# Kernel optimization log

Hardware: AMD Instinct MI355X
Metric: run time of the kernel (lower is better)

The kernel has to match this reference:

```python
import jax, jax.numpy as jnp
import numpy as np

D_MODEL = 1024
NUM_HEADS = 16
D_K = D_MODEL // NUM_HEADS


def setup_inputs() -> dict:
    key = jax.random.key(0)
    ks = jax.random.split(key, 12)
    B, S, D = 2, 2048, D_MODEL
    s = 1.0 / np.sqrt(D)
    inp = {
        "Q": jax.random.normal(ks[0], (B, S, D), jnp.float32),
        "K": jax.random.normal(ks[1], (B, S, D), jnp.float32),
        "V": jax.random.normal(ks[2], (B, S, D), jnp.float32),
        "Wq": jax.random.normal(ks[3], (D, D), jnp.float32) * s,
        "bq": jax.random.normal(ks[4], (D,), jnp.float32) * s,
        "Wk": jax.random.normal(ks[5], (D, D), jnp.float32) * s,
        "bk": jax.random.normal(ks[6], (D,), jnp.float32) * s,
        "Wv": jax.random.normal(ks[7], (D, D), jnp.float32) * s,
        "bv": jax.random.normal(ks[8], (D,), jnp.float32) * s,
        "Wo": jax.random.normal(ks[9], (D, D), jnp.float32) * s,
        "bo": jax.random.normal(ks[10], (D,), jnp.float32) * s,
    }
    return inp


def _split_heads(x, B, S):
    # [B, S, D] -> [B, H, S, d_k]
    return x.reshape(B, S, NUM_HEADS, D_K).transpose(0, 2, 1, 3)


def reference(Q, K, V, Wq, bq, Wk, bk, Wv, bv, Wo, bo):
    B, S, D = Q.shape
    # torch nn.Linear: y = x @ W.T + b
    q = _split_heads(Q @ Wq.T + bq, B, S)
    k = _split_heads(K @ Wk.T + bk, B, S)
    v = _split_heads(V @ Wv.T + bv, B, S)
    scale = 1.0 / np.sqrt(D_K).astype(np.float32)
    # [B, H, S, S] attention scores (materialized, as in the original)
    scores = jnp.einsum('bhqd,bhkd->bhqk', q, k) * scale
    probs = jax.nn.softmax(scores, axis=-1)
    out = jnp.einsum('bhqk,bhkd->bhqd', probs, v)
    out = out.transpose(0, 2, 1, 3).reshape(B, S, D)
    return out @ Wo.T + bo
```

## Files before the change

kernel.cpp:

```cpp
#include <hip/hip_runtime.h>
#include <hip/hip_bf16.h>

#define S_LEN   2048
#define NHEADS  16
#define DKH     64
#define DMODEL  1024
#define NBATCH  2

typedef __bf16 bf16x8 __attribute__((ext_vector_type(8)));
typedef __bf16 bf16x4 __attribute__((ext_vector_type(4)));
typedef float  f32x4  __attribute__((ext_vector_type(4)));

typedef __attribute__((address_space(3))) void       lds_void;
typedef const __attribute__((address_space(1))) void glob_void;

__device__ __forceinline__ void glds16(const void* g, void* l) {
    __builtin_amdgcn_global_load_lds((glob_void*)g, (lds_void*)l, 16, 0, 0);
}

struct CvtArgs {
    const float* src[7];
    __bf16*      dst[7];
    int          n[7];
};

__global__ __launch_bounds__(256)
void cvt_all_k(CvtArgs a)
{
    const int t = blockIdx.y;
    const size_t i = ((size_t)blockIdx.x * 256 + threadIdx.x) * 8;
    if ((int)i >= a.n[t]) return;
    const float* s = a.src[t];
    f32x4 lo = *(const f32x4*)(s + i);
    f32x4 hi = *(const f32x4*)(s + i + 4);
    bf16x8 r;
#pragma unroll
    for (int k = 0; k < 4; ++k) { r[k] = (__bf16)lo[k]; r[4 + k] = (__bf16)hi[k]; }
    *(bf16x8*)(a.dst[t] + i) = r;
}

#define BM 128
#define BN 64
#define BK 32

template<int MODE>
__global__ __launch_bounds__(256)
void gemm_tiled(const __bf16* __restrict__ A, const __bf16* __restrict__ W,
                const float* __restrict__ bias, void* __restrict__ outp,
                int M, int N, int K, float oscale)
{
    __shared__ __align__(16) __bf16 As[BM][BK];
    __shared__ __align__(16) __bf16 Ws[BN][BK];

    const int tid  = threadIdx.x;
    const int lane = tid & 63;
    const int wv   = tid >> 6;
    const int l15  = lane & 15;
    const int quad = lane >> 4;
    const int wm   = wv >> 1;
    const int wn   = wv & 1;

    const int fid = blockIdx.x;
    const int x  = fid & 7;
    const int j  = fid >> 3;
    const int m0 = (x * 4 + (j & 3)) * BM;
    const int n0 = (j >> 2) * BN;

    const int grow = lane >> 2;
    const int gcol = (lane & 3) * 8;
    const __bf16* ag0 = A + (size_t)(m0 + wv * 32 + grow) * K + gcol;
    const __bf16* ag1 = A + (size_t)(m0 + wv * 32 + 16 + grow) * K + gcol;
    const __bf16* wg  = W + (size_t)(n0 + wv * 16 + grow) * K + gcol;
    void* al0 = &As[wv * 32][0];
    void* al1 = &As[wv * 32 + 16][0];
    void* wl  = &Ws[wv * 16][0];

    f32x4 acc[4][2];
#pragma unroll
    for (int i = 0; i < 4; ++i)
#pragma unroll
        for (int jj = 0; jj < 2; ++jj) acc[i][jj] = (f32x4){0.f, 0.f, 0.f, 0.f};

    for (int k0 = 0;;) {
        __syncthreads();
        glds16(ag0 + k0, al0);
        glds16(ag1 + k0, al1);
        glds16(wg + k0, wl);
        __syncthreads();

        bf16x8 af[4], wf[2];
#pragma unroll
        for (int i = 0; i < 4; ++i)
            af[i] = *(const bf16x8*)&As[wm * 64 + i * 16 + l15][quad * 8];
#pragma unroll
        for (int jj = 0; jj < 2; ++jj)
            wf[jj] = *(const bf16x8*)&Ws[wn * 32 + jj * 16 + l15][quad * 8];
#pragma unroll
        for (int i = 0; i < 4; ++i)
#pragma unroll
            for (int jj = 0; jj < 2; ++jj)
                acc[i][jj] = __builtin_amdgcn_mfma_f32_16x16x32_bf16(af[i], wf[jj], acc[i][jj], 0, 0, 0);

        k0 += BK;
        if (k0 >= K) break;
    }

#pragma unroll
    for (int jj = 0; jj < 2; ++jj) {
        const int col = n0 + wn * 32 + jj * 16 + l15;
        const float bv = bias[col];
#pragma unroll
        for (int i = 0; i < 4; ++i) {
#pragma unroll
            for (int r = 0; r < 4; ++r) {
                const int row = m0 + wm * 64 + i * 16 + quad * 4 + r;
                const float v = (acc[i][jj][r] + bv) * oscale;
                if (MODE == 2) {
                    ((float*)outp)[(size_t)row * N + col] = v;
                } else {
                    const int b = row >> 11;
                    const int s = row & (S_LEN - 1);
                    const int h = col >> 6;
                    const int d = col & (DKH - 1);
                    const size_t idx = (MODE == 0)
                        ? ((size_t)(b * NHEADS + h) * S_LEN + s) * DKH + d
                        : ((size_t)(b * NHEADS + h) * DKH + d) * S_LEN + s;
                    ((__bf16*)outp)[idx] = (__bf16)v;
                }
            }
        }
    }
}

__global__ __launch_bounds__(512)
void attn_k(const __bf16* __restrict__ Qh, const __bf16* __restrict__ Kh,
            const __bf16* __restrict__ VhT, __bf16* __restrict__ out)
{
    __shared__ __align__(16) __bf16 Ks[64][72];
    __shared__ __align__(16) __bf16 Vs[64][72];

    const int tid  = threadIdx.x;
    const int lane = tid & 63;
    const int wv   = tid >> 6;
    const int l15  = lane & 15;
    const int quad = lane >> 4;

    const int fid = blockIdx.x;
    const int x  = fid & 7;
    const int j  = fid >> 3;
    const int bh = x * 4 + (j & 3);
    const int q0 = (j >> 2) * 128;
    const int b  = bh >> 4;
    const int h  = bh & (NHEADS - 1);

    const __bf16* Q  = Qh  + (size_t)bh * S_LEN * DKH;
    const __bf16* Kp = Kh  + (size_t)bh * S_LEN * DKH;
    const __bf16* Vt = VhT + (size_t)bh * DKH * S_LEN;

    const int qrow = q0 + wv * 16 + l15;
    const bf16x8 qa0 = *(const bf16x8*)(Q + (size_t)qrow * DKH + quad * 8);
    const bf16x8 qa1 = *(const bf16x8*)(Q + (size_t)qrow * DKH + quad * 8 + 32);

    const int srow = tid >> 3;
    const int scol = (tid & 7) * 8;
    const __bf16* kst = Kp + (size_t)srow * DKH   + scol;
    const __bf16* vst = Vt + (size_t)srow * S_LEN + scol;

    f32x4 oT[4];
#pragma unroll
    for (int jj = 0; jj < 4; ++jj) oT[jj] = (f32x4){0.f, 0.f, 0.f, 0.f};
    float lacc = 0.f;

    bf16x8 kr = *(const bf16x8*)(kst);
    bf16x8 vr = *(const bf16x8*)(vst);

    for (int kt = 0; kt < S_LEN; kt += 64) {
        __syncthreads();
        *(bf16x8*)&Ks[srow][scol] = kr;
        *(bf16x8*)&Vs[srow][scol] = vr;
        __syncthreads();
        if (kt + 64 < S_LEN) {
            kr = *(const bf16x8*)(kst + (size_t)(kt + 64) * DKH);
            vr = *(const bf16x8*)(vst + kt + 64);
        }

        float p[4][4];
#pragma unroll
        for (int n = 0; n < 4; ++n) {
            bf16x8 kA = *(const bf16x8*)&Ks[n * 16 + l15][quad * 8];
            bf16x8 kB = *(const bf16x8*)&Ks[n * 16 + l15][quad * 8 + 32];
            f32x4 st = {0.f, 0.f, 0.f, 0.f};
            st = __builtin_amdgcn_mfma_f32_16x16x32_bf16(kA, qa0, st, 0, 0, 0);
            st = __builtin_amdgcn_mfma_f32_16x16x32_bf16(kB, qa1, st, 0, 0, 0);
#pragma unroll
            for (int r = 0; r < 4; ++r) p[n][r] = __expf(st[r]);
        }
#pragma unroll
        for (int n = 0; n < 4; ++n)
#pragma unroll
            for (int r = 0; r < 4; ++r) lacc += p[n][r];

#pragma unroll
        for (int t = 0; t < 2; ++t) {
            bf16x8 pf;
#pragma unroll
            for (int jj = 0; jj < 4; ++jj) {
                pf[jj]     = (__bf16)p[2 * t][jj];
                pf[4 + jj] = (__bf16)p[2 * t + 1][jj];
            }
#pragma unroll
            for (int jt = 0; jt < 4; ++jt) {
                bf16x4 v0 = *(const bf16x4*)&Vs[jt * 16 + l15][t * 32 + quad * 4];
                bf16x4 v1 = *(const bf16x4*)&Vs[jt * 16 + l15][t * 32 + 16 + quad * 4];
                bf16x8 vf;
#pragma unroll
                for (int jj = 0; jj < 4; ++jj) { vf[jj] = v0[jj]; vf[4 + jj] = v1[jj]; }
                oT[jt] = __builtin_amdgcn_mfma_f32_16x16x32_bf16(vf, pf, oT[jt], 0, 0, 0);
            }
        }
    }

    lacc += __shfl_xor(lacc, 16);
    lacc += __shfl_xor(lacc, 32);
    const float inv = 1.0f / lacc;

    __bf16* op = out + ((size_t)b * S_LEN + q0 + wv * 16 + l15) * DMODEL + h * DKH;
#pragma unroll
    for (int jt = 0; jt < 4; ++jt)
#pragma unroll
        for (int r = 0; r < 4; ++r)
            op[jt * 16 + quad * 4 + r] = (__bf16)(oT[jt][r] * inv);
}

extern "C" void kernel_launch(void* const* d_in, const int* in_sizes, int n_in,
                              void* d_out, int out_size, void* d_ws, size_t ws_size,
                              hipStream_t stream) {
    const float* Qi = (const float*)d_in[0];
    const float* Ki = (const float*)d_in[1];
    const float* Vi = (const float*)d_in[2];
    const float* Wq = (const float*)d_in[3];
    const float* bq = (const float*)d_in[4];
    const float* Wk = (const float*)d_in[5];
    const float* bk = (const float*)d_in[6];
    const float* Wv = (const float*)d_in[7];
    const float* bv = (const float*)d_in[8];
    const float* Wo = (const float*)d_in[9];
    const float* bo = (const float*)d_in[10];
    float* out = (float*)d_out;

    const int M = NBATCH * S_LEN;
    const size_t NW = (size_t)DMODEL * DMODEL;
    const size_t NE = (size_t)M * DMODEL;
    __bf16* w_bf   = (__bf16*)d_ws;
    __bf16* Qin_bf = w_bf + 4 * NW;
    __bf16* Kin_bf = Qin_bf + NE;
    __bf16* Vin_bf = Kin_bf + NE;
    __bf16* q_ws   = Vin_bf + NE;
    __bf16* k_ws   = q_ws + NE;
    __bf16* vT_ws   = Kin_bf;
    __bf16* attn_ws = Qin_bf;
    __bf16* wq_bf = w_bf, *wk_bf = w_bf + NW, *wv_bf = w_bf + 2 * NW, *wo_bf = w_bf + 3 * NW;

    CvtArgs ca;
    ca.src[0] = Wq; ca.src[1] = Wk; ca.src[2] = Wv; ca.src[3] = Wo;
    ca.src[4] = Qi; ca.src[5] = Ki; ca.src[6] = Vi;
    ca.dst[0] = wq_bf; ca.dst[1] = wk_bf; ca.dst[2] = wv_bf; ca.dst[3] = wo_bf;
    ca.dst[4] = Qin_bf; ca.dst[5] = Kin_bf; ca.dst[6] = Vin_bf;
    for (int t = 0; t < 4; ++t) ca.n[t] = (int)NW;
    for (int t = 4; t < 7; ++t) ca.n[t] = (int)NE;
    cvt_all_k<<<dim3(2048, 7), 256, 0, stream>>>(ca);

    dim3 blk(256);
    dim3 ggrid(512);
    gemm_tiled<0><<<ggrid, blk, 0, stream>>>(Qin_bf, wq_bf, bq, q_ws,  M, DMODEL, DMODEL, 0.125f);
    gemm_tiled<0><<<ggrid, blk, 0, stream>>>(Kin_bf, wk_bf, bk, k_ws,  M, DMODEL, DMODEL, 1.0f);
    gemm_tiled<1><<<ggrid, blk, 0, stream>>>(Vin_bf, wv_bf, bv, vT_ws, M, DMODEL, DMODEL, 1.0f);

    attn_k<<<dim3(512), dim3(512), 0, stream>>>(q_ws, k_ws, vT_ws, attn_ws);

    gemm_tiled<2><<<ggrid, blk, 0, stream>>>(attn_ws, wo_bf, bo, out, M, DMODEL, DMODEL, 1.0f);
}
```

Measured before the change: 256.5 us.

## Batch QKV GEMMs into one launch, enlarge GEMM tiles, widen attention K/V tiles

```diff
diff --git a/kernel.cpp b/kernel.cpp
--- a/kernel.cpp
+++ b/kernel.cpp
@@ -39,19 +39,11 @@
     *(bf16x8*)(a.dst[t] + i) = r;
 }
 
-#define BM 128
-#define BN 64
-#define BK 32
-
-template<int MODE>
-__global__ __launch_bounds__(256)
-void gemm_tiled(const __bf16* __restrict__ A, const __bf16* __restrict__ W,
-                const float* __restrict__ bias, void* __restrict__ outp,
-                int M, int N, int K, float oscale)
-{
-    __shared__ __align__(16) __bf16 As[BM][BK];
-    __shared__ __align__(16) __bf16 Ws[BN][BK];
-
+__device__ __forceinline__ void gemm_core(
+    const __bf16* __restrict__ A, const __bf16* __restrict__ W,
+    int m0, int n0, int K,
+    __bf16 (*As)[32], __bf16 (*Ws)[32], f32x4 acc[4][4])
+{
     const int tid  = threadIdx.x;
     const int lane = tid & 63;
     const int wv   = tid >> 6;
@@ -59,76 +51,147 @@
     const int quad = lane >> 4;
     const int wm   = wv >> 1;
     const int wn   = wv & 1;
-
-    const int fid = blockIdx.x;
-    const int x  = fid & 7;
-    const int j  = fid >> 3;
-    const int m0 = (x * 4 + (j & 3)) * BM;
-    const int n0 = (j >> 2) * BN;
-
     const int grow = lane >> 2;
     const int gcol = (lane & 3) * 8;
+
     const __bf16* ag0 = A + (size_t)(m0 + wv * 32 + grow) * K + gcol;
     const __bf16* ag1 = A + (size_t)(m0 + wv * 32 + 16 + grow) * K + gcol;
-    const __bf16* wg  = W + (size_t)(n0 + wv * 16 + grow) * K + gcol;
+    const __bf16* wg0 = W + (size_t)(n0 + wv * 32 + grow) * K + gcol;
+    const __bf16* wg1 = W + (size_t)(n0 + wv * 32 + 16 + grow) * K + gcol;
     void* al0 = &As[wv * 32][0];
     void* al1 = &As[wv * 32 + 16][0];
-    void* wl  = &Ws[wv * 16][0];
-
-    f32x4 acc[4][2];
-#pragma unroll
-    for (int i = 0; i < 4; ++i)
-#pragma unroll
-        for (int jj = 0; jj < 2; ++jj) acc[i][jj] = (f32x4){0.f, 0.f, 0.f, 0.f};
+    void* wl0 = &Ws[wv * 32][0];
+    void* wl1 = &Ws[wv * 32 + 16][0];
 
     for (int k0 = 0;;) {
         __syncthreads();
         glds16(ag0 + k0, al0);
         glds16(ag1 + k0, al1);
-        glds16(wg + k0, wl);
+        glds16(wg0 + k0, wl0);
+        glds16(wg1 + k0, wl1);
         __syncthreads();
 
-        bf16x8 af[4], wf[2];
+        bf16x8 af[4], wf[4];
 #pragma unroll
         for (int i = 0; i < 4; ++i)
             af[i] = *(const bf16x8*)&As[wm * 64 + i * 16 + l15][quad * 8];
 #pragma unroll
-        for (int jj = 0; jj < 2; ++jj)
-            wf[jj] = *(const bf16x8*)&Ws[wn * 32 + jj * 16 + l15][quad * 8];
+        for (int j = 0; j < 4; ++j)
+            wf[j] = *(const bf16x8*)&Ws[wn * 64 + j * 16 + l15][quad * 8];
 #pragma unroll
         for (int i = 0; i < 4; ++i)
 #pragma unroll
-            for (int jj = 0; jj < 2; ++jj)
-                acc[i][jj] = __builtin_amdgcn_mfma_f32_16x16x32_bf16(af[i], wf[jj], acc[i][jj], 0, 0, 0);
-
-        k0 += BK;
+            for (int j = 0; j < 4; ++j)
+                acc[i][j] = __builtin_amdgcn_mfma_f32_16x16x32_bf16(af[i], wf[j], acc[i][j], 0, 0, 0);
+
+        k0 += 32;
         if (k0 >= K) break;
     }
-
-#pragma unroll
-    for (int jj = 0; jj < 2; ++jj) {
-        const int col = n0 + wn * 32 + jj * 16 + l15;
-        const float bv = bias[col];
+}
+
+struct GArgs {
+    const __bf16* A[3];
+    const __bf16* W[3];
+    const float*  bias[3];
+    __bf16*       out[3];
+};
+
+__global__ __launch_bounds__(256)
+void gemm_qkv(GArgs g, int z_off)
+{
+    __shared__ __align__(16) __bf16 As[128][32];
+    __shared__ __align__(16) __bf16 Ws[128][32];
+
+    const int fid = blockIdx.x;
+    const int z   = (fid >> 8) + z_off;
+    const int f8  = fid & 255;
+    int m0, n0;
+    if (z == 2) { m0 = (f8 & 7) * 128;  n0 = (f8 >> 3) * 128; }
+    else        { m0 = (f8 & 31) * 128; n0 = (f8 >> 5) * 128; }
+
+    f32x4 acc[4][4];
+#pragma unroll
+    for (int i = 0; i < 4; ++i)
+#pragma unroll
+        for (int j = 0; j < 4; ++j) acc[i][j] = (f32x4){0.f, 0.f, 0.f, 0.f};
+
+    gemm_core(g.A[z], g.W[z], m0, n0, DMODEL, As, Ws, acc);
+
+    const int lane = threadIdx.x & 63;
+    const int wv   = threadIdx.x >> 6;
+    const int l15  = lane & 15;
+    const int quad = lane >> 4;
+    const int wm   = wv >> 1;
+    const int wn   = wv & 1;
+    const float* bias = g.bias[z];
+    __bf16* out = g.out[z];
+    const float oscale = (z == 0) ? 0.125f : 1.0f;
+
+#pragma unroll
+    for (int j = 0; j < 4; ++j) {
+        const int col = n0 + wn * 64 + j * 16 + l15;
+        const float bcol = (z == 2) ? 0.f : bias[col];
 #pragma unroll
         for (int i = 0; i < 4; ++i) {
 #pragma unroll
             for (int r = 0; r < 4; ++r) {
                 const int row = m0 + wm * 64 + i * 16 + quad * 4 + r;
-                const float v = (acc[i][jj][r] + bv) * oscale;
-                if (MODE == 2) {
-                    ((float*)outp)[(size_t)row * N + col] = v;
+                size_t idx;
+                float v = acc[i][j][r];
+                if (z == 2) {
+                    const int h = row >> 6, d = row & (DKH - 1);
+                    const int b = col >> 11, s = col & (S_LEN - 1);
+                    v += bias[row];
+                    idx = ((size_t)(b * NHEADS + h) * DKH + d) * S_LEN + s;
                 } else {
-                    const int b = row >> 11;
-                    const int s = row & (S_LEN - 1);
-                    const int h = col >> 6;
-                    const int d = col & (DKH - 1);
-                    const size_t idx = (MODE == 0)
-                        ? ((size_t)(b * NHEADS + h) * S_LEN + s) * DKH + d
-                        : ((size_t)(b * NHEADS + h) * DKH + d) * S_LEN + s;
-                    ((__bf16*)outp)[idx] = (__bf16)v;
+                    const int b = row >> 11, s = row & (S_LEN - 1);
+                    const int h = col >> 6, d = col & (DKH - 1);
+                    v = (v + bcol) * oscale;
+                    idx = ((size_t)(b * NHEADS + h) * S_LEN + s) * DKH + d;
                 }
+                out[idx] = (__bf16)v;
             }
         }
+    }
+}
+
+__global__ __launch_bounds__(256)
+void gemm_out(const __bf16* __restrict__ A, const __bf16* __restrict__ W,
+              const float* __restrict__ bias, float* __restrict__ out)
+{
+    __shared__ __align__(16) __bf16 As[128][32];
+    __shared__ __align__(16) __bf16 Ws[128][32];
+
+    const int fid = blockIdx.x;
+    const int m0 = (fid & 31) * 128;
+    const int n0 = (fid >> 5) * 128;
+
+    f32x4 acc[4][4];
+#pragma unroll
+    for (int i = 0; i < 4; ++i)
+#pragma unroll
+        for (int j = 0; j < 4; ++j) acc[i][j] = (f32x4){0.f, 0.f, 0.f, 0.f};
+
+    gemm_core(A, W, m0, n0, DMODEL, As, Ws, acc);
+
+    const int lane = threadIdx.x & 63;
+    const int wv   = threadIdx.x >> 6;
+    const int l15  = lane & 15;
+    const int quad = lane >> 4;
+    const int wm   = wv >> 1;
+    const int wn   = wv & 1;
+
+#pragma unroll
+    for (int j = 0; j < 4; ++j) {
+        const int col = n0 + wn * 64 + j * 16 + l15;
+        const float bv = bias[col];
+#pragma unroll
+        for (int i = 0; i < 4; ++i)
+#pragma unroll
+            for (int r = 0; r < 4; ++r) {
+                const int row = m0 + wm * 64 + i * 16 + quad * 4 + r;
+                out[(size_t)row * DMODEL + col] = acc[i][j][r] + bv;
+            }
     }
 }
 
@@ -136,8 +199,8 @@
 void attn_k(const __bf16* __restrict__ Qh, const __bf16* __restrict__ Kh,
             const __bf16* __restrict__ VhT, __bf16* __restrict__ out)
 {
-    __shared__ __align__(16) __bf16 Ks[64][72];
-    __shared__ __align__(16) __bf16 Vs[64][72];
+    __shared__ __align__(16) __bf16 Ks[128][72];
+    __shared__ __align__(16) __bf16 Vs[64][136];
 
     const int tid  = threadIdx.x;
     const int lane = tid & 63;
@@ -161,61 +224,72 @@
     const bf16x8 qa0 = *(const bf16x8*)(Q + (size_t)qrow * DKH + quad * 8);
     const bf16x8 qa1 = *(const bf16x8*)(Q + (size_t)qrow * DKH + quad * 8 + 32);
 
-    const int srow = tid >> 3;
-    const int scol = (tid & 7) * 8;
-    const __bf16* kst = Kp + (size_t)srow * DKH   + scol;
-    const __bf16* vst = Vt + (size_t)srow * S_LEN + scol;
+    const int krow = tid >> 2;
+    const int kc0  = (tid & 3) * 16;
+    const int vrow = tid >> 3;
+    const int vc0  = (tid & 7) * 16;
+    const __bf16* kst = Kp + (size_t)krow * DKH   + kc0;
+    const __bf16* vst = Vt + (size_t)vrow * S_LEN + vc0;
 
     f32x4 oT[4];
 #pragma unroll
     for (int jj = 0; jj < 4; ++jj) oT[jj] = (f32x4){0.f, 0.f, 0.f, 0.f};
     float lacc = 0.f;
 
-    bf16x8 kr = *(const bf16x8*)(kst);
-    bf16x8 vr = *(const bf16x8*)(vst);
-
-    for (int kt = 0; kt < S_LEN; kt += 64) {
+    bf16x8 ka = *(const bf16x8*)(kst);
+    bf16x8 kb = *(const bf16x8*)(kst + 8);
+    bf16x8 va = *(const bf16x8*)(vst);
+    bf16x8 vb = *(const bf16x8*)(vst + 8);
+
+    for (int kt = 0; kt < S_LEN; kt += 128) {
         __syncthreads();
-        *(bf16x8*)&Ks[srow][scol] = kr;
-        *(bf16x8*)&Vs[srow][scol] = vr;
+        *(bf16x8*)&Ks[krow][kc0]     = ka;
+        *(bf16x8*)&Ks[krow][kc0 + 8] = kb;
+        *(bf16x8*)&Vs[vrow][vc0]     = va;
+        *(bf16x8*)&Vs[vrow][vc0 + 8] = vb;
         __syncthreads();
-        if (kt + 64 < S_LEN) {
-            kr = *(const bf16x8*)(kst + (size_t)(kt + 64) * DKH);
-            vr = *(const bf16x8*)(vst + kt + 64);
+        if (kt + 128 < S_LEN) {
+            ka = *(const bf16x8*)(kst + (size_t)(kt + 128) * DKH);
+            kb = *(const bf16x8*)(kst + (size_t)(kt + 128) * DKH + 8);
+            va = *(const bf16x8*)(vst + kt + 128);
+            vb = *(const bf16x8*)(vst + kt + 128 + 8);
         }
 
-        float p[4][4];
-#pragma unroll
-        for (int n = 0; n < 4; ++n) {
-            bf16x8 kA = *(const bf16x8*)&Ks[n * 16 + l15][quad * 8];
-            bf16x8 kB = *(const bf16x8*)&Ks[n * 16 + l15][quad * 8 + 32];
-            f32x4 st = {0.f, 0.f, 0.f, 0.f};
-            st = __builtin_amdgcn_mfma_f32_16x16x32_bf16(kA, qa0, st, 0, 0, 0);
-            st = __builtin_amdgcn_mfma_f32_16x16x32_bf16(kB, qa1, st, 0, 0, 0);
-#pragma unroll
-            for (int r = 0; r < 4; ++r) p[n][r] = __expf(st[r]);
-        }
-#pragma unroll
-        for (int n = 0; n < 4; ++n)
-#pragma unroll
-            for (int r = 0; r < 4; ++r) lacc += p[n][r];
-
-#pragma unroll
-        for (int t = 0; t < 2; ++t) {
-            bf16x8 pf;
-#pragma unroll
-            for (int jj = 0; jj < 4; ++jj) {
-                pf[jj]     = (__bf16)p[2 * t][jj];
-                pf[4 + jj] = (__bf16)p[2 * t + 1][jj];
+#pragma unroll
+        for (int ht = 0; ht < 2; ++ht) {
+            float p[4][4];
+#pragma unroll
+            for (int n = 0; n < 4; ++n) {
+                bf16x8 kA = *(const bf16x8*)&Ks[ht * 64 + n * 16 + l15][quad * 8];
+                bf16x8 kB = *(const bf16x8*)&Ks[ht * 64 + n * 16 + l15][quad * 8 + 32];
+                f32x4 st = {0.f, 0.f, 0.f, 0.f};
+                st = __builtin_amdgcn_mfma_f32_16x16x32_bf16(kA, qa0, st, 0, 0, 0);
+                st = __builtin_amdgcn_mfma_f32_16x16x32_bf16(kB, qa1, st, 0, 0, 0);
+#pragma unroll
+                for (int r = 0; r < 4; ++r) p[n][r] = __expf(st[r]);
             }
 #pragma unroll
-            for (int jt = 0; jt < 4; ++jt) {
-                bf16x4 v0 = *(const bf16x4*)&Vs[jt * 16 + l15][t * 32 + quad * 4];
-                bf16x4 v1 = *(const bf16x4*)&Vs[jt * 16 + l15][t * 32 + 16 + quad * 4];
-                bf16x8 vf;
-#pragma unroll
-                for (int jj = 0; jj < 4; ++jj) { vf[jj] = v0[jj]; vf[4 + jj] = v1[jj]; }
-                oT[jt] = __builtin_amdgcn_mfma_f32_16x16x32_bf16(vf, pf, oT[jt], 0, 0, 0);
+            for (int n = 0; n < 4; ++n)
+#pragma unroll
+                for (int r = 0; r < 4; ++r) lacc += p[n][r];
+
+#pragma unroll
+            for (int t = 0; t < 2; ++t) {
+                bf16x8 pf;
+#pragma unroll
+                for (int jj = 0; jj < 4; ++jj) {
+                    pf[jj]     = (__bf16)p[2 * t][jj];
+                    pf[4 + jj] = (__bf16)p[2 * t + 1][jj];
+                }
+#pragma unroll
+                for (int jt = 0; jt < 4; ++jt) {
+                    bf16x4 v0 = *(const bf16x4*)&Vs[jt * 16 + l15][ht * 64 + t * 32 + quad * 4];
+                    bf16x4 v1 = *(const bf16x4*)&Vs[jt * 16 + l15][ht * 64 + t * 32 + 16 + quad * 4];
+                    bf16x8 vf;
+#pragma unroll
+                    for (int jj = 0; jj < 4; ++jj) { vf[jj] = v0[jj]; vf[4 + jj] = v1[jj]; }
+                    oT[jt] = __builtin_amdgcn_mfma_f32_16x16x32_bf16(vf, pf, oT[jt], 0, 0, 0);
+                }
             }
         }
     }
@@ -226,10 +300,12 @@
 
     __bf16* op = out + ((size_t)b * S_LEN + q0 + wv * 16 + l15) * DMODEL + h * DKH;
 #pragma unroll
-    for (int jt = 0; jt < 4; ++jt)
-#pragma unroll
-        for (int r = 0; r < 4; ++r)
-            op[jt * 16 + quad * 4 + r] = (__bf16)(oT[jt][r] * inv);
+    for (int jt = 0; jt < 4; ++jt) {
+        bf16x4 t;
+#pragma unroll
+        for (int r = 0; r < 4; ++r) t[r] = (__bf16)(oT[jt][r] * inv);
+        *(bf16x4*)(op + jt * 16 + quad * 4) = t;
+    }
 }
 
 extern "C" void kernel_launch(void* const* d_in, const int* in_sizes, int n_in,
@@ -251,13 +327,15 @@
     const int M = NBATCH * S_LEN;
     const size_t NW = (size_t)DMODEL * DMODEL;
     const size_t NE = (size_t)M * DMODEL;
+    const bool big = ws_size >= ((size_t)56 << 20);
+
     __bf16* w_bf   = (__bf16*)d_ws;
     __bf16* Qin_bf = w_bf + 4 * NW;
     __bf16* Kin_bf = Qin_bf + NE;
     __bf16* Vin_bf = Kin_bf + NE;
     __bf16* q_ws   = Vin_bf + NE;
     __bf16* k_ws   = q_ws + NE;
-    __bf16* vT_ws   = Kin_bf;
+    __bf16* vT_ws   = big ? (k_ws + NE) : Kin_bf;
     __bf16* attn_ws = Qin_bf;
     __bf16* wq_bf = w_bf, *wk_bf = w_bf + NW, *wv_bf = w_bf + 2 * NW, *wo_bf = w_bf + 3 * NW;
 
@@ -270,13 +348,18 @@
     for (int t = 4; t < 7; ++t) ca.n[t] = (int)NE;
     cvt_all_k<<<dim3(2048, 7), 256, 0, stream>>>(ca);
 
-    dim3 blk(256);
-    dim3 ggrid(512);
-    gemm_tiled<0><<<ggrid, blk, 0, stream>>>(Qin_bf, wq_bf, bq, q_ws,  M, DMODEL, DMODEL, 0.125f);
-    gemm_tiled<0><<<ggrid, blk, 0, stream>>>(Kin_bf, wk_bf, bk, k_ws,  M, DMODEL, DMODEL, 1.0f);
-    gemm_tiled<1><<<ggrid, blk, 0, stream>>>(Vin_bf, wv_bf, bv, vT_ws, M, DMODEL, DMODEL, 1.0f);
+    GArgs g;
+    g.A[0] = Qin_bf; g.W[0] = wq_bf; g.bias[0] = bq; g.out[0] = q_ws;
+    g.A[1] = Kin_bf; g.W[1] = wk_bf; g.bias[1] = bk; g.out[1] = k_ws;
+    g.A[2] = wv_bf;  g.W[2] = Vin_bf; g.bias[2] = bv; g.out[2] = vT_ws;
+    if (big) {
+        gemm_qkv<<<dim3(768), 256, 0, stream>>>(g, 0);
+    } else {
+        gemm_qkv<<<dim3(512), 256, 0, stream>>>(g, 0);
+        gemm_qkv<<<dim3(256), 256, 0, stream>>>(g, 2);
+    }
 
     attn_k<<<dim3(512), dim3(512), 0, stream>>>(q_ws, k_ws, vT_ws, attn_ws);
 
-    gemm_tiled<2><<<ggrid, blk, 0, stream>>>(attn_ws, wo_bf, bo, out, M, DMODEL, DMODEL, 1.0f);
-}
+    gemm_out<<<dim3(256), 256, 0, stream>>>(attn_ws, wo_bf, bo, out);
+}
```

New measurement: 235.3 us. 8.3% less time.
